# Kernel tuning notes

Measured on AMD Instinct MI355X. Metric: run time of the kernel, lower is better.

The kernel has to match this reference:

```python
import jax, jax.numpy as jnp
import numpy as np

C = 256; M = 8; K = 4; L = 4; DFF = 1024; CV = C // M
SHAPES = [(100, 100), (50, 50), (25, 25), (13, 13)]
B = 16; LQ = 900


def setup_inputs() -> dict:
    key = jax.random.key(0)
    ks = iter(jax.random.split(key, 64))
    def n(shape, s=0.02):
        return jax.random.normal(next(ks), shape, jnp.float32) * s
    inp = {
        "query_objects": n((LQ, B, C), 1.0),
        "query_poses": n((LQ, B, C), 1.0),
        "ref_points": jax.random.uniform(next(ks), (LQ, B, 2), jnp.float32),
    }
    for i, (h, w) in enumerate(SHAPES):
        inp[f"feat{i}"] = n((B, h, w, C), 1.0)
        inp[f"pos{i}"] = n((B, h, w, C), 1.0)
    inp.update(dict(
        sa_in_w=n((C, 3 * C)), sa_in_b=jnp.zeros((3 * C,), jnp.float32),
        sa_out_w=n((C, C)), sa_out_b=jnp.zeros((C,), jnp.float32),
        n1_g=jnp.ones((C,), jnp.float32), n1_b=jnp.zeros((C,), jnp.float32),
        n2_g=jnp.ones((C,), jnp.float32), n2_b=jnp.zeros((C,), jnp.float32),
        n3_g=jnp.ones((C,), jnp.float32), n3_b=jnp.zeros((C,), jnp.float32),
        val_w=n((C, C)), val_b=jnp.zeros((C,), jnp.float32),
        off_w=n((C, M * L * K * 2)), off_b=n((M * L * K * 2,), 0.5),
        aw_w=n((C, M * L * K)), aw_b=jnp.zeros((M * L * K,), jnp.float32),
        dout_w=n((C, C)), dout_b=jnp.zeros((C,), jnp.float32),
        ffn_w1=n((C, DFF)), ffn_b1=jnp.zeros((DFF,), jnp.float32),
        ffn_w2=n((DFF, C)), ffn_b2=jnp.zeros((C,), jnp.float32),
    ))
    return inp


def layernorm(x, g, b, eps=1e-5):
    m = x.mean(-1, keepdims=True)
    v = ((x - m) ** 2).mean(-1, keepdims=True)
    return (x - m) * jax.lax.rsqrt(v + eps) * g + b


def mha(x_q, x_k, x_v, Win, bin_, Wout, bout):
    # torch nn.MultiheadAttention, seq-first (Lq, B, C), no masks, eval mode
    Lq, Bn, _ = x_q.shape
    q = (x_q @ Win[:, :C] + bin_[:C]).reshape(Lq, Bn, M, CV)
    k = (x_k @ Win[:, C:2 * C] + bin_[C:2 * C]).reshape(Lq, Bn, M, CV)
    v = (x_v @ Win[:, 2 * C:] + bin_[2 * C:]).reshape(Lq, Bn, M, CV)
    a = jax.nn.softmax(jnp.einsum('qbmd,kbmd->bmqk', q * (CV ** -0.5), k), axis=-1)
    o = jnp.einsum('bmqk,kbmd->qbmd', a, v).reshape(Lq, Bn, C)
    return o @ Wout + bout


def deform_attn(qd, ref, feats, val_w, val_b, off_w, off_b, aw_w, aw_b, dout_w, dout_b):
    # qd: (B, Lq, C) queries; ref: (B, Lq, 2) normalized [0,1] reference points (x, y)
    Bn, Lq, _ = qd.shape
    off = (qd @ off_w + off_b).reshape(Bn, Lq, M, L, K, 2)            # sampling offsets (pixels)
    aw = jax.nn.softmax((qd @ aw_w + aw_b).reshape(Bn, Lq, M, L * K), axis=-1)
    aw = aw.reshape(Bn, Lq, M, L, K)                                   # attention weights over L*K
    out = jnp.zeros((Bn, Lq, M, CV), qd.dtype)
    for l, feat in enumerate(feats):
        H, W = feat.shape[1], feat.shape[2]
        # shared value projection, split into heads: (B, M, HW, Cv)
        v = (feat.reshape(Bn, H * W, C) @ val_w + val_b).reshape(Bn, H * W, M, CV).transpose(0, 2, 1, 3)
        px = ref[:, :, None, None, 0] * W - 0.5 + off[:, :, :, l, :, 0]  # (B, Lq, M, K)
        py = ref[:, :, None, None, 1] * H - 0.5 + off[:, :, :, l, :, 1]
        x0 = jnp.floor(px); y0 = jnp.floor(py)
        samp = jnp.zeros((Bn, M, Lq, K, CV), qd.dtype)
        for dx in (0.0, 1.0):
            for dy in (0.0, 1.0):
                xi = x0 + dx; yi = y0 + dy
                wgt = (1.0 - jnp.abs(px - xi)) * (1.0 - jnp.abs(py - yi))
                valid = (xi >= 0) & (xi < W) & (yi >= 0) & (yi < H)      # zero padding outside
                idx = (jnp.clip(yi, 0, H - 1) * W + jnp.clip(xi, 0, W - 1)).astype(jnp.int32)
                idx_t = idx.transpose(0, 2, 1, 3).reshape(Bn, M, Lq * K)
                g = jnp.take_along_axis(v, idx_t[..., None], axis=2).reshape(Bn, M, Lq, K, CV)
                samp = samp + g * (wgt * valid).transpose(0, 2, 1, 3)[..., None]
        out = out + jnp.einsum('bqmk,bmqkc->bqmc', aw[:, :, :, l], samp)
    return out.reshape(Bn, Lq, C) @ dout_w + dout_b


def reference(query_objects, query_poses, ref_points, feat0, feat1, feat2, feat3,
              pos0, pos1, pos2, pos3, sa_in_w, sa_in_b, sa_out_w, sa_out_b,
              n1_g, n1_b, n2_g, n2_b, n3_g, n3_b, val_w, val_b, off_w, off_b,
              aw_w, aw_b, dout_w, dout_b, ffn_w1, ffn_b1, ffn_w2, ffn_b2):
    # post-norm decoder layer, eval mode (dropout = identity)
    q = query_objects + query_poses
    x = query_objects + mha(q, q, query_objects, sa_in_w, sa_in_b, sa_out_w, sa_out_b)
    x = layernorm(x, n1_g, n1_b)
    feats = [feat0 + pos0, feat1 + pos1, feat2 + pos2, feat3 + pos3]
    qd = x.transpose(1, 0, 2)              # (B, Lq, C)
    ref = ref_points.transpose(1, 0, 2)    # (B, Lq, 2)
    d = deform_attn(qd, ref, feats, val_w, val_b, off_w, off_b, aw_w, aw_b, dout_w, dout_b)
    x = x + d.transpose(1, 0, 2)
    x = layernorm(x, n2_g, n2_b)
    x = x + (jax.nn.relu(x @ ffn_w1 + ffn_b1) @ ffn_w2 + ffn_b2)
    x = layernorm(x, n3_g, n3_b)
    return x
```

## Files before the change

kernel.cpp:

```cpp
#include <hip/hip_runtime.h>
#include <hip/hip_bf16.h>
#include <cstdint>

#define LQ 900
#define BB 16
#define CC 256
#define MM 8
#define CV 32
#define NROWS (LQ * BB)

typedef __attribute__((ext_vector_type(8))) short short8;
typedef __attribute__((ext_vector_type(4))) float f32x4;

__device__ __forceinline__ short f2bf(float f) {
    union { float f; unsigned u; } x; x.f = f;
    const unsigned r = x.u + 0x7fff + ((x.u >> 16) & 1);
    return (short)(r >> 16);
}
__device__ __forceinline__ float bf2f(ushort u) {
    union { unsigned u; float f; } c; c.u = ((unsigned)u) << 16; return c.f;
}

__device__ __constant__ int d_HW[4]    = {100, 50, 25, 13};
__device__ __constant__ int d_baseR[4] = {0, 160000, 200000, 210000};

__global__ __launch_bounds__(256) void conv_w_T(
    const float* __restrict__ W, ushort* __restrict__ Wt, int K, int N)
{
    __shared__ float tl[32][33];
    const int t = threadIdx.x;
    const int tx = t & 31, ty = t >> 5;
    const int n0 = blockIdx.x * 32, k0 = blockIdx.y * 32;
    #pragma unroll
    for (int p = 0; p < 4; ++p)
        tl[ty + 8 * p][tx] = W[(size_t)(k0 + ty + 8 * p) * N + n0 + tx];
    __syncthreads();
    #pragma unroll
    for (int p = 0; p < 4; ++p)
        Wt[(size_t)(n0 + ty + 8 * p) * K + k0 + tx] = (ushort)f2bf(tl[tx][ty + 8 * p]);
}

__global__ void concat_bias(const float* __restrict__ a, const float* __restrict__ b,
                            float* __restrict__ o)
{
    const int t = blockIdx.x * 256 + threadIdx.x;
    if (t < 384) o[t] = (t < 256) ? a[t] : b[t - 256];
}

#define EPS 136
#define LDSN 17408

template<bool A_BF16, bool ADD_A2, bool RELU, bool RESID, bool OUT_BF16>
__device__ __forceinline__ void gemm_core(
    ushort* lds,
    const void* __restrict__ Ap, const float* __restrict__ A2, int lda,
    const ushort* __restrict__ Bt, const float* __restrict__ bias,
    const float* __restrict__ resid, void* __restrict__ Cp, int ldc,
    int Mr, int Kd, int row0, int col0)
{
    ushort* As = lds;
    ushort* Bs = lds + 8192;

    const int t = threadIdx.x;
    const int lane = t & 63;
    const int w = t >> 6;
    const int wr = w >> 1, wc = w & 1;
    const int lr = lane & 15, lk = lane >> 4;

    f32x4 acc[4][4] = {};

    const int srow = t >> 4;
    const int skq  = (t & 15) * 4;
    const int sg   = (t & 15) >> 1;
    const int srem = (t & 1) * 8;

    const float*  Af = (const float*)Ap;
    const ushort* Ah = (const ushort*)Ap;

    short4 sa_[8], sb_[8];
    float4 fa_[8], f2_[8];

    const int nk = Kd >> 6;

    auto issue = [&](int kk0) {
        #pragma unroll
        for (int p = 0; p < 8; ++p) {
            const int gr = min(row0 + p * 16 + srow, Mr - 1);
            if constexpr (A_BF16) {
                sa_[p] = *reinterpret_cast<const short4*>(Ah + (size_t)gr * lda + kk0 + skq);
            } else {
                fa_[p] = *reinterpret_cast<const float4*>(Af + (size_t)gr * lda + kk0 + skq);
                if constexpr (ADD_A2)
                    f2_[p] = *reinterpret_cast<const float4*>(A2 + (size_t)gr * lda + kk0 + skq);
            }
            sb_[p] = *reinterpret_cast<const short4*>(Bt + (size_t)(col0 + p * 16 + srow) * Kd + kk0 + skq);
        }
    };

    issue(0);

    for (int kt = 0; kt < nk; ++kt) {
        #pragma unroll
        for (int p = 0; p < 8; ++p) {
            const int r = p * 16 + srow;
            short4 a4;
            if constexpr (A_BF16) {
                a4 = sa_[p];
            } else {
                float4 av = fa_[p];
                if constexpr (ADD_A2) {
                    av.x += f2_[p].x; av.y += f2_[p].y; av.z += f2_[p].z; av.w += f2_[p].w;
                }
                a4.x = f2bf(av.x); a4.y = f2bf(av.y); a4.z = f2bf(av.z); a4.w = f2bf(av.w);
            }
            const int byteA = r * 128 + ((sg ^ (r & 7)) << 4) + srem;
            *reinterpret_cast<short4*>((char*)As + byteA) = a4;
            *reinterpret_cast<short4*>((char*)Bs + byteA) = sb_[p];
        }
        __syncthreads();

        if (kt + 1 < nk) issue((kt + 1) * 64);

        #pragma unroll
        for (int kk = 0; kk < 2; ++kk) {
            short8 af[4], bfr[4];
            #pragma unroll
            for (int i = 0; i < 4; ++i) {
                const int r = wr * 64 + i * 16 + lr;
                const int byte = r * 128 + (((kk * 4 + lk) ^ (r & 7)) << 4);
                af[i] = *reinterpret_cast<const short8*>((char*)As + byte);
            }
            #pragma unroll
            for (int j = 0; j < 4; ++j) {
                const int r = wc * 64 + j * 16 + lr;
                const int byte = r * 128 + (((kk * 4 + lk) ^ (r & 7)) << 4);
                bfr[j] = *reinterpret_cast<const short8*>((char*)Bs + byte);
            }
            #pragma unroll
            for (int i = 0; i < 4; ++i)
                #pragma unroll
                for (int j = 0; j < 4; ++j)
                    acc[i][j] = __builtin_amdgcn_mfma_f32_16x16x32_bf16(af[i], bfr[j], acc[i][j], 0, 0, 0);
        }
        __syncthreads();
    }

    if constexpr (OUT_BF16) {
        ushort* Cb = (ushort*)Cp;
        #pragma unroll
        for (int j = 0; j < 4; ++j) {
            const int lcol = wc * 64 + j * 16 + lr;
            const float bcol = bias[col0 + lcol];
            #pragma unroll
            for (int i = 0; i < 4; ++i) {
                const int lrbase = wr * 64 + i * 16 + lk * 4;
                #pragma unroll
                for (int reg = 0; reg < 4; ++reg) {
                    float v = acc[i][j][reg] + bcol;
                    if (RELU) v = fmaxf(v, 0.f);
                    lds[(lrbase + reg) * EPS + lcol] = (ushort)f2bf(v);
                }
            }
        }
        __syncthreads();
        const int erow = t >> 1, ehalf = t & 1;
        if (row0 + erow < Mr) {
            ushort* dst = Cb + (size_t)(row0 + erow) * ldc + col0 + ehalf * 64;
            const ushort* src = lds + erow * EPS + ehalf * 64;
            #pragma unroll
            for (int q = 0; q < 8; ++q)
                *reinterpret_cast<short8*>(dst + q * 8) =
                    *reinterpret_cast<const short8*>(src + q * 8);
        }
    } else {
        float* Cf = (float*)Cp;
        #pragma unroll
        for (int j = 0; j < 4; ++j) {
            const int col = col0 + wc * 64 + j * 16 + lr;
            const float bcol = bias[col];
            #pragma unroll
            for (int i = 0; i < 4; ++i) {
                const int rbase = row0 + wr * 64 + i * 16 + lk * 4;
                #pragma unroll
                for (int reg = 0; reg < 4; ++reg) {
                    const int r = rbase + reg;
                    if (r < Mr) {
                        float v = acc[i][j][reg] + bcol;
                        if (RESID) v += resid[(size_t)r * ldc + col];
                        if (RELU)  v = fmaxf(v, 0.f);
                        Cf[(size_t)r * ldc + col] = v;
                    }
                }
            }
        }
    }
}

template<bool A_BF16, bool ADD_A2, bool RELU, bool RESID, bool OUT_BF16>
__global__ __launch_bounds__(256) void gemm_bf16(
    const void* __restrict__ Ap, const float* __restrict__ A2, int lda,
    const ushort* __restrict__ Bt, const float* __restrict__ bias,
    const float* __restrict__ resid, void* __restrict__ Cp, int ldc,
    int Mr, int Kd)
{
    __shared__ ushort lds[LDSN];
    gemm_core<A_BF16, ADD_A2, RELU, RESID, OUT_BF16>(
        lds, Ap, A2, lda, Bt, bias, resid, Cp, ldc, Mr, Kd,
        blockIdx.y * 128, blockIdx.x * 128);
}

__global__ __launch_bounds__(256) void attn_mfma(
    const ushort* __restrict__ QKbf, const ushort* __restrict__ Vbf,
    ushort* __restrict__ attnO)
{
    __shared__ ushort K_lds[64][40];
    __shared__ ushort Vt[32][72];
    __shared__ ushort P_lds[4][16][72];

    const int t = threadIdx.x;
    const int w = t >> 6, lane = t & 63;
    const int q0 = blockIdx.x * 64;
    const int m = blockIdx.y & 7, b = blockIdx.y >> 3;

    const int lr = lane & 15;
    const int lk = lane >> 4;

    const int qrow = min(q0 + w * 16 + lr, LQ - 1);
    const short8 qf = *reinterpret_cast<const short8*>(
        QKbf + ((size_t)qrow * BB + b) * 512 + m * 32 + lk * 8);

    f32x4 oacc[2] = {f32x4{0.f,0.f,0.f,0.f}, f32x4{0.f,0.f,0.f,0.f}};
    float mrun[4] = {-1e30f, -1e30f, -1e30f, -1e30f};
    float lrun[4] = {0.f, 0.f, 0.f, 0.f};

    const float scale = 0.17677669529663687f;
    const int sr = t >> 2;
    const int sd = (t & 3) * 8;

    for (int k0 = 0; k0 < LQ; k0 += 64) {
        {
            const int kr = min(k0 + sr, LQ - 1);
            *reinterpret_cast<short8*>(&K_lds[sr][sd]) =
                *reinterpret_cast<const short8*>(QKbf + ((size_t)kr * BB + b) * 512 + 256 + m * 32 + sd);
            const short8 v8 = *reinterpret_cast<const short8*>(
                Vbf + ((size_t)kr * BB + b) * 256 + m * 32 + sd);
            #pragma unroll
            for (int j = 0; j < 8; ++j) Vt[sd + j][sr] = (ushort)v8[j];
        }
        __syncthreads();

        f32x4 sa[4];
        #pragma unroll
        for (int n = 0; n < 4; ++n) {
            const short8 kf = *reinterpret_cast<const short8*>(&K_lds[n * 16 + lr][lk * 8]);
            sa[n] = __builtin_amdgcn_mfma_f32_16x16x32_bf16(qf, kf, f32x4{0.f,0.f,0.f,0.f}, 0, 0, 0);
        }
        #pragma unroll
        for (int n = 0; n < 4; ++n)
            #pragma unroll
            for (int r = 0; r < 4; ++r)
                sa[n][r] *= scale;
        if (k0 + 64 > LQ) {
            #pragma unroll
            for (int n = 0; n < 4; ++n)
                if (k0 + n * 16 + lr >= LQ) {
                    #pragma unroll
                    for (int r = 0; r < 4; ++r) sa[n][r] = -1e30f;
                }
        }

        #pragma unroll
        for (int r = 0; r < 4; ++r) {
            float mx = fmaxf(fmaxf(sa[0][r], sa[1][r]), fmaxf(sa[2][r], sa[3][r]));
            #pragma unroll
            for (int o = 8; o; o >>= 1) mx = fmaxf(mx, __shfl_xor(mx, o));
            const float mnew = fmaxf(mrun[r], mx);
            const float corr = __expf(mrun[r] - mnew);
            mrun[r] = mnew;
            float psum = 0.f;
            #pragma unroll
            for (int n = 0; n < 4; ++n) {
                const float p = __expf(sa[n][r] - mnew);
                psum += p;
                P_lds[w][lk * 4 + r][n * 16 + lr] = (ushort)f2bf(p);
            }
            #pragma unroll
            for (int o = 8; o; o >>= 1) psum += __shfl_xor(psum, o);
            lrun[r] = lrun[r] * corr + psum;
            oacc[0][r] *= corr;
            oacc[1][r] *= corr;
        }

        #pragma unroll
        for (int kk = 0; kk < 2; ++kk) {
            const short8 pf = *reinterpret_cast<const short8*>(&P_lds[w][lr][kk * 32 + lk * 8]);
            #pragma unroll
            for (int dt = 0; dt < 2; ++dt) {
                const short8 vf = *reinterpret_cast<const short8*>(&Vt[dt * 16 + lr][kk * 32 + lk * 8]);
                oacc[dt] = __builtin_amdgcn_mfma_f32_16x16x32_bf16(pf, vf, oacc[dt], 0, 0, 0);
            }
        }
        __syncthreads();
    }

    #pragma unroll
    for (int r = 0; r < 4; ++r) {
        const int row = q0 + w * 16 + lk * 4 + r;
        if (row < LQ) {
            const float inv = 1.f / lrun[r];
            ushort* op = attnO + ((size_t)row * BB + b) * 256 + m * 32;
            op[lr]      = (ushort)f2bf(oacc[0][r] * inv);
            op[16 + lr] = (ushort)f2bf(oacc[1][r] * inv);
        }
    }
}

__global__ __launch_bounds__(256) void ln_kernel(
    const float* __restrict__ X, const float* __restrict__ g,
    const float* __restrict__ bta, float* __restrict__ Y, int nrows)
{
    const int r = blockIdx.x * 4 + (threadIdx.x >> 6);
    if (r >= nrows) return;
    const int lane = threadIdx.x & 63;
    const float4 v = *reinterpret_cast<const float4*>(X + (size_t)r * 256 + lane * 4);
    float s  = v.x + v.y + v.z + v.w;
    float sq = v.x * v.x + v.y * v.y + v.z * v.z + v.w * v.w;
    #pragma unroll
    for (int o = 32; o; o >>= 1) { s += __shfl_xor(s, o); sq += __shfl_xor(sq, o); }
    const float mean = s * (1.f / 256.f);
    const float var  = sq * (1.f / 256.f) - mean * mean;
    const float rs   = rsqrtf(var + 1e-5f);
    const float4 gv = *reinterpret_cast<const float4*>(g + lane * 4);
    const float4 bv = *reinterpret_cast<const float4*>(bta + lane * 4);
    float4 o4;
    o4.x = (v.x - mean) * rs * gv.x + bv.x;
    o4.y = (v.y - mean) * rs * gv.y + bv.y;
    o4.z = (v.z - mean) * rs * gv.z + bv.z;
    o4.w = (v.w - mean) * rs * gv.w + bv.w;
    *reinterpret_cast<float4*>(Y + (size_t)r * 256 + lane * 4) = o4;
}

__global__ __launch_bounds__(256) void samp_prep(
    const float* __restrict__ ref, const float* __restrict__ obf,
    int4* __restrict__ prepI, float4* __restrict__ prepW)
{
    const int gid = blockIdx.x * 256 + threadIdx.x;
    const int k = gid & 3, l = (gid >> 2) & 3, m = (gid >> 4) & 7, row = gid >> 7;
    const int b = row & 15;

    const float logit = obf[(size_t)row * 384 + 256 + m * 16 + l * 4 + k];
    float mx = logit;
    #pragma unroll
    for (int o = 1; o < 16; o <<= 1) mx = fmaxf(mx, __shfl_xor(mx, o));
    const float e = __expf(logit - mx);
    float se = e;
    #pragma unroll
    for (int o = 1; o < 16; o <<= 1) se += __shfl_xor(se, o);
    const float aw = e / se;

    const int   Hl = d_HW[l];
    const float Hf = (float)Hl;
    const int   gbase = d_baseR[l] + b * Hl * Hl;
    const float rx = ref[row * 2 + 0], ry = ref[row * 2 + 1];
    const float ox = obf[(size_t)row * 384 + m * 32 + l * 8 + k * 2 + 0];
    const float oy = obf[(size_t)row * 384 + m * 32 + l * 8 + k * 2 + 1];
    const float px = rx * Hf - 0.5f + ox;
    const float py = ry * Hf - 0.5f + oy;
    const float x0 = floorf(px), y0 = floorf(py);

    int4 I; float4 W;
    #pragma unroll
    for (int c = 0; c < 4; ++c) {
        const float xi = x0 + (float)(c & 1);
        const float yi = y0 + (float)(c >> 1);
        const float wv = (1.f - fabsf(px - xi)) * (1.f - fabsf(py - yi));
        const bool valid = (xi >= 0.f) && (xi < Hf) && (yi >= 0.f) && (yi < Hf);
        const int ix = min(max((int)xi, 0), Hl - 1);
        const int iy = min(max((int)yi, 0), Hl - 1);
        const int idx = gbase + iy * Hl + ix;
        const float wgt = valid ? aw * wv : 0.f;
        if (c == 0) { I.x = idx; W.x = wgt; }
        else if (c == 1) { I.y = idx; W.y = wgt; }
        else if (c == 2) { I.z = idx; W.z = wgt; }
        else { I.w = idx; W.w = wgt; }
    }
    prepI[gid] = I;
    prepW[gid] = W;
}

__global__ __launch_bounds__(256) void samp_gather(
    const ushort* __restrict__ Vval, const int4* __restrict__ prepI,
    const float4* __restrict__ prepW, float* __restrict__ samp)
{
    const int wid  = blockIdx.x * 4 + (threadIdx.x >> 6);
    const int lane = threadIdx.x & 63;
    const int q  = wid % LQ;
    const int bm = wid / LQ;
    const int m  = bm & 7, b = bm >> 3;
    const int row = q * BB + b;
    const int sid = lane >> 3, dg = lane & 7;

    const uint2* V4 = (const uint2*)Vval;
    const int pbase = (row * 8 + m) * 16;
    const int coff  = m * 8 + dg;

    float a0 = 0.f, a1 = 0.f, a2 = 0.f, a3 = 0.f;
    #pragma unroll
    for (int g = 0; g < 2; ++g) {
        const int s = g * 8 + sid;
        const int4   I = prepI[pbase + s];
        const float4 W = prepW[pbase + s];
        uint2 v;
        v = V4[(size_t)I.x * 64 + coff];
        a0 += W.x * bf2f((ushort)v.x); a1 += W.x * bf2f((ushort)(v.x >> 16));
        a2 += W.x * bf2f((ushort)v.y); a3 += W.x * bf2f((ushort)(v.y >> 16));
        v = V4[(size_t)I.y * 64 + coff];
        a0 += W.y * bf2f((ushort)v.x); a1 += W.y * bf2f((ushort)(v.x >> 16));
        a2 += W.y * bf2f((ushort)v.y); a3 += W.y * bf2f((ushort)(v.y >> 16));
        v = V4[(size_t)I.z * 64 + coff];
        a0 += W.z * bf2f((ushort)v.x); a1 += W.z * bf2f((ushort)(v.x >> 16));
        a2 += W.z * bf2f((ushort)v.y); a3 += W.z * bf2f((ushort)(v.y >> 16));
        v = V4[(size_t)I.w * 64 + coff];
        a0 += W.w * bf2f((ushort)v.x); a1 += W.w * bf2f((ushort)(v.x >> 16));
        a2 += W.w * bf2f((ushort)v.y); a3 += W.w * bf2f((ushort)(v.y >> 16));
    }
    #pragma unroll
    for (int o = 8; o <= 32; o <<= 1) {
        a0 += __shfl_xor(a0, o); a1 += __shfl_xor(a1, o);
        a2 += __shfl_xor(a2, o); a3 += __shfl_xor(a3, o);
    }
    if (sid == 0) {
        float4 o4; o4.x = a0; o4.y = a1; o4.z = a2; o4.w = a3;
        *reinterpret_cast<float4*>(samp + (size_t)row * 256 + m * 32 + dg * 4) = o4;
    }
}

extern "C" void kernel_launch(void* const* d_in, const int* in_sizes, int n_in,
                              void* d_out, int out_size, void* d_ws, size_t ws_size,
                              hipStream_t stream)
{
    const float* qo   = (const float*)d_in[0];
    const float* qpz  = (const float*)d_in[1];
    const float* refp = (const float*)d_in[2];
    const float* feat[4] = {(const float*)d_in[3], (const float*)d_in[5],
                            (const float*)d_in[7], (const float*)d_in[9]};
    const float* pos[4]  = {(const float*)d_in[4], (const float*)d_in[6],
                            (const float*)d_in[8], (const float*)d_in[10]};
    const float* sa_in_w  = (const float*)d_in[11];
    const float* sa_in_b  = (const float*)d_in[12];
    const float* sa_out_w = (const float*)d_in[13];
    const float* sa_out_b = (const float*)d_in[14];
    const float* n1_g = (const float*)d_in[15];
    const float* n1_b = (const float*)d_in[16];
    const float* n2_g = (const float*)d_in[17];
    const float* n2_b = (const float*)d_in[18];
    const float* n3_g = (const float*)d_in[19];
    const float* n3_b = (const float*)d_in[20];
    const float* val_w  = (const float*)d_in[21];
    const float* val_b  = (const float*)d_in[22];
    const float* off_w  = (const float*)d_in[23];
    const float* off_b  = (const float*)d_in[24];
    const float* aw_w   = (const float*)d_in[25];
    const float* aw_b   = (const float*)d_in[26];
    const float* dout_w = (const float*)d_in[27];
    const float* dout_b = (const float*)d_in[28];
    const float* ffn_w1 = (const float*)d_in[29];
    const float* ffn_b1 = (const float*)d_in[30];
    const float* ffn_w2 = (const float*)d_in[31];
    const float* ffn_b2 = (const float*)d_in[32];

    char* ws = (char*)d_ws;
    ushort* QKbf   = (ushort*)(ws + 0);
    ushort* Vbf    = (ushort*)(ws + 14745600);
    ushort* attnO  = (ushort*)(ws + 22118400);
    ushort* Vval   = (ushort*)(ws + 29491200);
    ushort* WsaInT = (ushort*)(ws + 138395648);
    ushort* WsaOutT= (ushort*)(ws + 138788864);
    ushort* WvalT  = (ushort*)(ws + 138919936);
    ushort* WdoutT = (ushort*)(ws + 139051008);
    ushort* Wffn1T = (ushort*)(ws + 139182080);
    ushort* Wffn2T = (ushort*)(ws + 139706368);
    ushort* WoffAwT= (ushort*)(ws + 140230656);
    float*  obias  = (float*)(ws + 140427264);
    float* x1   = (float*)(ws + 140429312);
    float* dres = x1;
    float* xln1 = (float*)(ws + 155174912);
    float* obf  = (float*)(ws + 169920512);
    float* x3   = obf;
    float* samp = (float*)(ws + 192038912);
    float* xln2 = (float*)(ws + 206784512);
    ushort* h   = (ushort*)(ws + 221530112);
    int4*  prepI = (int4*)(ws + 251021312);
    float4* prepW = (float4*)(ws + 280512512);

    const dim3 blk(256);
    const int GM = (NROWS + 127) / 128;

    conv_w_T<<<dim3(24, 8), blk, 0, stream>>>(sa_in_w, WsaInT, 256, 768);
    conv_w_T<<<dim3(8, 8), blk, 0, stream>>>(sa_out_w, WsaOutT, 256, 256);
    conv_w_T<<<dim3(8, 8), blk, 0, stream>>>(val_w, WvalT, 256, 256);
    conv_w_T<<<dim3(8, 8), blk, 0, stream>>>(dout_w, WdoutT, 256, 256);
    conv_w_T<<<dim3(32, 8), blk, 0, stream>>>(ffn_w1, Wffn1T, 256, 1024);
    conv_w_T<<<dim3(8, 32), blk, 0, stream>>>(ffn_w2, Wffn2T, 1024, 256);
    conv_w_T<<<dim3(8, 8), blk, 0, stream>>>(off_w, WoffAwT, 256, 256);
    conv_w_T<<<dim3(4, 8), blk, 0, stream>>>(aw_w, WoffAwT + 256 * 256, 256, 128);
    concat_bias<<<dim3(2), blk, 0, stream>>>(off_b, aw_b, obias);

    gemm_bf16<false, true, false, false, true><<<dim3(4, GM), blk, 0, stream>>>(
        qo, qpz, 256, WsaInT, sa_in_b, nullptr, QKbf, 512, NROWS, 256);
    gemm_bf16<false, false, false, false, true><<<dim3(2, GM), blk, 0, stream>>>(
        qo, nullptr, 256, WsaInT + 512 * 256, sa_in_b + 512, nullptr, Vbf, 256, NROWS, 256);
    attn_mfma<<<dim3(15, 128), blk, 0, stream>>>(QKbf, Vbf, attnO);
    gemm_bf16<true, false, false, true, false><<<dim3(2, GM), blk, 0, stream>>>(
        attnO, nullptr, 256, WsaOutT, sa_out_b, qo, x1, 256, NROWS, 256);
    ln_kernel<<<dim3(3600), blk, 0, stream>>>(x1, n1_g, n1_b, xln1, NROWS);
    gemm_bf16<false, false, false, false, false><<<dim3(3, GM), blk, 0, stream>>>(
        xln1, nullptr, 256, WoffAwT, obias, nullptr, obf, 384, NROWS, 256);
    samp_prep<<<dim3(7200), blk, 0, stream>>>(refp, obf, prepI, prepW);
    gemm_bf16<false, true, false, false, true><<<dim3(2, 1250), blk, 0, stream>>>(
        feat[0], pos[0], 256, WvalT, val_b, nullptr, Vval, 256, 160000, 256);
    gemm_bf16<false, true, false, false, true><<<dim3(2, 313), blk, 0, stream>>>(
        feat[1], pos[1], 256, WvalT, val_b, nullptr, Vval + (size_t)160000 * 256, 256, 40000, 256);
    gemm_bf16<false, true, false, false, true><<<dim3(2, 79), blk, 0, stream>>>(
        feat[2], pos[2], 256, WvalT, val_b, nullptr, Vval + (size_t)200000 * 256, 256, 10000, 256);
    gemm_bf16<false, true, false, false, true><<<dim3(2, 22), blk, 0, stream>>>(
        feat[3], pos[3], 256, WvalT, val_b, nullptr, Vval + (size_t)210000 * 256, 256, 2704, 256);
    samp_gather<<<dim3(28800), blk, 0, stream>>>(Vval, prepI, prepW, samp);
    gemm_bf16<false, false, false, true, false><<<dim3(2, GM), blk, 0, stream>>>(
        samp, nullptr, 256, WdoutT, dout_b, xln1, dres, 256, NROWS, 256);
    ln_kernel<<<dim3(3600), blk, 0, stream>>>(dres, n2_g, n2_b, xln2, NROWS);
    gemm_bf16<false, false, true, false, true><<<dim3(8, GM), blk, 0, stream>>>(
        xln2, nullptr, 256, Wffn1T, ffn_b1, nullptr, h, 1024, NROWS, 256);
    gemm_bf16<true, false, false, true, false><<<dim3(2, GM), blk, 0, stream>>>(
        h, nullptr, 1024, Wffn2T, ffn_b2, xln2, x3, 256, NROWS, 1024);
    ln_kernel<<<dim3(3600), blk, 0, stream>>>(x3, n3_g, n3_b, (float*)d_out, NROWS);
}
```

Before: 600.0 us.

## Merge weight conversion launches, fuse sampling prep into gather, store intermediates in bf16

All weight transpose/convert launches and the bias concat are folded into one kernel that looks up its work item through a packed descriptor. The sampling-prep kernel is removed: each gather wavefront now computes its own softmax weights and bilinear indices into LDS, so the prepI/prepW buffers no longer go through global memory. LayerNorm outputs and the sampled features are stored as bf16, and the downstream GEMMs read bf16 A operands and bf16 residuals. This cuts launch count and global traffic, at the cost of extra rounding on the residual paths.

New measurement: 529.2 us. 1.13x faster.

```diff
diff --git a/kernel.cpp b/kernel.cpp
--- a/kernel.cpp
+++ b/kernel.cpp
@@ -24,38 +24,57 @@
 __device__ __constant__ int d_HW[4]    = {100, 50, 25, 13};
 __device__ __constant__ int d_baseR[4] = {0, 160000, 200000, 210000};
 
-__global__ __launch_bounds__(256) void conv_w_T(
-    const float* __restrict__ W, ushort* __restrict__ Wt, int K, int N)
-{
+struct WPack {
+    const float* W[8];
+    ushort*      Wt[8];
+    int K[8];
+    int N[8];
+    int cum[9];
+    const float* offb;
+    const float* awb;
+    float*       obias;
+};
+
+__global__ __launch_bounds__(256) void conv_all(WPack p)
+{
+    const int bb = blockIdx.x;
+    if (bb == p.cum[8]) {
+        for (int t = threadIdx.x; t < 384; t += 256)
+            p.obias[t] = (t < 256) ? p.offb[t] : p.awb[t - 256];
+        return;
+    }
+    int wi = 0;
+    #pragma unroll
+    for (int i = 0; i < 8; ++i)
+        if (bb >= p.cum[i + 1]) wi = i + 1;
+    const int ti  = bb - p.cum[wi];
+    const int N   = p.N[wi], K = p.K[wi];
+    const int ntx = N >> 5;
+    const int n0  = (ti % ntx) * 32, k0 = (ti / ntx) * 32;
+    const float* W  = p.W[wi];
+    ushort*      Wt = p.Wt[wi];
+
     __shared__ float tl[32][33];
     const int t = threadIdx.x;
     const int tx = t & 31, ty = t >> 5;
-    const int n0 = blockIdx.x * 32, k0 = blockIdx.y * 32;
-    #pragma unroll
-    for (int p = 0; p < 4; ++p)
-        tl[ty + 8 * p][tx] = W[(size_t)(k0 + ty + 8 * p) * N + n0 + tx];
+    #pragma unroll
+    for (int q = 0; q < 4; ++q)
+        tl[ty + 8 * q][tx] = W[(size_t)(k0 + ty + 8 * q) * N + n0 + tx];
     __syncthreads();
     #pragma unroll
-    for (int p = 0; p < 4; ++p)
-        Wt[(size_t)(n0 + ty + 8 * p) * K + k0 + tx] = (ushort)f2bf(tl[tx][ty + 8 * p]);
-}
-
-__global__ void concat_bias(const float* __restrict__ a, const float* __restrict__ b,
-                            float* __restrict__ o)
-{
-    const int t = blockIdx.x * 256 + threadIdx.x;
-    if (t < 384) o[t] = (t < 256) ? a[t] : b[t - 256];
+    for (int q = 0; q < 4; ++q)
+        Wt[(size_t)(n0 + ty + 8 * q) * K + k0 + tx] = (ushort)f2bf(tl[tx][ty + 8 * q]);
 }
 
 #define EPS 136
 #define LDSN 17408
 
-template<bool A_BF16, bool ADD_A2, bool RELU, bool RESID, bool OUT_BF16>
+template<bool A_BF16, bool ADD_A2, bool RELU, bool RESID, bool RESID_BF16, bool OUT_BF16>
 __device__ __forceinline__ void gemm_core(
     ushort* lds,
     const void* __restrict__ Ap, const float* __restrict__ A2, int lda,
     const ushort* __restrict__ Bt, const float* __restrict__ bias,
-    const float* __restrict__ resid, void* __restrict__ Cp, int ldc,
+    const void* __restrict__ resid, void* __restrict__ Cp, int ldc,
     int Mr, int Kd, int row0, int col0)
 {
     ushort* As = lds;
@@ -186,8 +205,13 @@
                     const int r = rbase + reg;
                     if (r < Mr) {
                         float v = acc[i][j][reg] + bcol;
-                        if (RESID) v += resid[(size_t)r * ldc + col];
-                        if (RELU)  v = fmaxf(v, 0.f);
+                        if (RESID) {
+                            if (RESID_BF16)
+                                v += bf2f(((const ushort*)resid)[(size_t)r * ldc + col]);
+                            else
+                                v += ((const float*)resid)[(size_t)r * ldc + col];
+                        }
+                        if (RELU) v = fmaxf(v, 0.f);
                         Cf[(size_t)r * ldc + col] = v;
                     }
                 }
@@ -196,15 +220,15 @@
     }
 }
 
-template<bool A_BF16, bool ADD_A2, bool RELU, bool RESID, bool OUT_BF16>
+template<bool A_BF16, bool ADD_A2, bool RELU, bool RESID, bool RESID_BF16, bool OUT_BF16>
 __global__ __launch_bounds__(256) void gemm_bf16(
     const void* __restrict__ Ap, const float* __restrict__ A2, int lda,
     const ushort* __restrict__ Bt, const float* __restrict__ bias,
-    const float* __restrict__ resid, void* __restrict__ Cp, int ldc,
+    const void* __restrict__ resid, void* __restrict__ Cp, int ldc,
     int Mr, int Kd)
 {
     __shared__ ushort lds[LDSN];
-    gemm_core<A_BF16, ADD_A2, RELU, RESID, OUT_BF16>(
+    gemm_core<A_BF16, ADD_A2, RELU, RESID, RESID_BF16, OUT_BF16>(
         lds, Ap, A2, lda, Bt, bias, resid, Cp, ldc, Mr, Kd,
         blockIdx.y * 128, blockIdx.x * 128);
 }
@@ -315,9 +339,10 @@
     }
 }
 
+template<bool OUT_BF16>
 __global__ __launch_bounds__(256) void ln_kernel(
     const float* __restrict__ X, const float* __restrict__ g,
-    const float* __restrict__ bta, float* __restrict__ Y, int nrows)
+    const float* __restrict__ bta, void* __restrict__ Y, int nrows)
 {
     const int r = blockIdx.x * 4 + (threadIdx.x >> 6);
     if (r >= nrows) return;
@@ -337,79 +362,75 @@
     o4.y = (v.y - mean) * rs * gv.y + bv.y;
     o4.z = (v.z - mean) * rs * gv.z + bv.z;
     o4.w = (v.w - mean) * rs * gv.w + bv.w;
-    *reinterpret_cast<float4*>(Y + (size_t)r * 256 + lane * 4) = o4;
-}
-
-__global__ __launch_bounds__(256) void samp_prep(
-    const float* __restrict__ ref, const float* __restrict__ obf,
-    int4* __restrict__ prepI, float4* __restrict__ prepW)
-{
-    const int gid = blockIdx.x * 256 + threadIdx.x;
-    const int k = gid & 3, l = (gid >> 2) & 3, m = (gid >> 4) & 7, row = gid >> 7;
-    const int b = row & 15;
-
-    const float logit = obf[(size_t)row * 384 + 256 + m * 16 + l * 4 + k];
-    float mx = logit;
-    #pragma unroll
-    for (int o = 1; o < 16; o <<= 1) mx = fmaxf(mx, __shfl_xor(mx, o));
-    const float e = __expf(logit - mx);
-    float se = e;
-    #pragma unroll
-    for (int o = 1; o < 16; o <<= 1) se += __shfl_xor(se, o);
-    const float aw = e / se;
-
-    const int   Hl = d_HW[l];
-    const float Hf = (float)Hl;
-    const int   gbase = d_baseR[l] + b * Hl * Hl;
-    const float rx = ref[row * 2 + 0], ry = ref[row * 2 + 1];
-    const float ox = obf[(size_t)row * 384 + m * 32 + l * 8 + k * 2 + 0];
-    const float oy = obf[(size_t)row * 384 + m * 32 + l * 8 + k * 2 + 1];
-    const float px = rx * Hf - 0.5f + ox;
-    const float py = ry * Hf - 0.5f + oy;
-    const float x0 = floorf(px), y0 = floorf(py);
-
-    int4 I; float4 W;
-    #pragma unroll
-    for (int c = 0; c < 4; ++c) {
-        const float xi = x0 + (float)(c & 1);
-        const float yi = y0 + (float)(c >> 1);
-        const float wv = (1.f - fabsf(px - xi)) * (1.f - fabsf(py - yi));
-        const bool valid = (xi >= 0.f) && (xi < Hf) && (yi >= 0.f) && (yi < Hf);
-        const int ix = min(max((int)xi, 0), Hl - 1);
-        const int iy = min(max((int)yi, 0), Hl - 1);
-        const int idx = gbase + iy * Hl + ix;
-        const float wgt = valid ? aw * wv : 0.f;
-        if (c == 0) { I.x = idx; W.x = wgt; }
-        else if (c == 1) { I.y = idx; W.y = wgt; }
-        else if (c == 2) { I.z = idx; W.z = wgt; }
-        else { I.w = idx; W.w = wgt; }
-    }
-    prepI[gid] = I;
-    prepW[gid] = W;
+    if (OUT_BF16) {
+        short4 u;
+        u.x = f2bf(o4.x); u.y = f2bf(o4.y); u.z = f2bf(o4.z); u.w = f2bf(o4.w);
+        *reinterpret_cast<short4*>((ushort*)Y + (size_t)r * 256 + lane * 4) = u;
+    } else {
+        *reinterpret_cast<float4*>((float*)Y + (size_t)r * 256 + lane * 4) = o4;
+    }
 }
 
 __global__ __launch_bounds__(256) void samp_gather(
-    const ushort* __restrict__ Vval, const int4* __restrict__ prepI,
-    const float4* __restrict__ prepW, float* __restrict__ samp)
-{
-    const int wid  = blockIdx.x * 4 + (threadIdx.x >> 6);
+    const ushort* __restrict__ Vval, const float* __restrict__ obf,
+    const float* __restrict__ ref, ushort* __restrict__ samp)
+{
+    __shared__ int   sI[4][16][4];
+    __shared__ float sW[4][16][4];
+
+    const int w    = threadIdx.x >> 6;
     const int lane = threadIdx.x & 63;
+    const int wid  = blockIdx.x * 4 + w;
     const int q  = wid % LQ;
     const int bm = wid / LQ;
     const int m  = bm & 7, b = bm >> 3;
     const int row = q * BB + b;
+
+    if (lane < 16) {
+        const float logit = obf[(size_t)row * 384 + 256 + m * 16 + lane];
+        float mx = logit;
+        #pragma unroll
+        for (int o = 1; o < 16; o <<= 1) mx = fmaxf(mx, __shfl_xor(mx, o));
+        const float e = __expf(logit - mx);
+        float se = e;
+        #pragma unroll
+        for (int o = 1; o < 16; o <<= 1) se += __shfl_xor(se, o);
+        const float aw = e / se;
+
+        const int   l  = lane >> 2;
+        const int   Hl = d_HW[l];
+        const float Hf = (float)Hl;
+        const int   gbase = d_baseR[l] + b * Hl * Hl;
+        const float rx = ref[row * 2 + 0], ry = ref[row * 2 + 1];
+        const float ox = obf[(size_t)row * 384 + m * 32 + lane * 2 + 0];
+        const float oy = obf[(size_t)row * 384 + m * 32 + lane * 2 + 1];
+        const float px = rx * Hf - 0.5f + ox;
+        const float py = ry * Hf - 0.5f + oy;
+        const float x0 = floorf(px), y0 = floorf(py);
+
+        #pragma unroll
+        for (int c = 0; c < 4; ++c) {
+            const float xi = x0 + (float)(c & 1);
+            const float yi = y0 + (float)(c >> 1);
+            const float wv = (1.f - fabsf(px - xi)) * (1.f - fabsf(py - yi));
+            const bool valid = (xi >= 0.f) && (xi < Hf) && (yi >= 0.f) && (yi < Hf);
+            const int ix = min(max((int)xi, 0), Hl - 1);
+            const int iy = min(max((int)yi, 0), Hl - 1);
+            sI[w][lane][c] = gbase + iy * Hl + ix;
+            sW[w][lane][c] = valid ? aw * wv : 0.f;
+        }
+    }
+
     const int sid = lane >> 3, dg = lane & 7;
-
     const uint2* V4 = (const uint2*)Vval;
-    const int pbase = (row * 8 + m) * 16;
     const int coff  = m * 8 + dg;
 
     float a0 = 0.f, a1 = 0.f, a2 = 0.f, a3 = 0.f;
     #pragma unroll
     for (int g = 0; g < 2; ++g) {
         const int s = g * 8 + sid;
-        const int4   I = prepI[pbase + s];
-        const float4 W = prepW[pbase + s];
+        const int4   I = *reinterpret_cast<const int4*>(&sI[w][s][0]);
+        const float4 W = *reinterpret_cast<const float4*>(&sW[w][s][0]);
         uint2 v;
         v = V4[(size_t)I.x * 64 + coff];
         a0 += W.x * bf2f((ushort)v.x); a1 += W.x * bf2f((ushort)(v.x >> 16));
@@ -430,8 +451,9 @@
         a2 += __shfl_xor(a2, o); a3 += __shfl_xor(a3, o);
     }
     if (sid == 0) {
-        float4 o4; o4.x = a0; o4.y = a1; o4.z = a2; o4.w = a3;
-        *reinterpret_cast<float4*>(samp + (size_t)row * 256 + m * 32 + dg * 4) = o4;
+        short4 u;
+        u.x = f2bf(a0); u.y = f2bf(a1); u.z = f2bf(a2); u.w = f2bf(a3);
+        *reinterpret_cast<short4*>(samp + (size_t)row * 256 + m * 32 + dg * 4) = u;
     }
 }
 
@@ -482,56 +504,57 @@
     ushort* Wffn2T = (ushort*)(ws + 139706368);
     ushort* WoffAwT= (ushort*)(ws + 140230656);
     float*  obias  = (float*)(ws + 140427264);
-    float* x1   = (float*)(ws + 140429312);
-    float* dres = x1;
-    float* xln1 = (float*)(ws + 155174912);
-    float* obf  = (float*)(ws + 169920512);
-    float* x3   = obf;
-    float* samp = (float*)(ws + 192038912);
-    float* xln2 = (float*)(ws + 206784512);
-    ushort* h   = (ushort*)(ws + 221530112);
-    int4*  prepI = (int4*)(ws + 251021312);
-    float4* prepW = (float4*)(ws + 280512512);
+    float*  x1   = (float*)(ws + 140429312);
+    float*  dres = x1;
+    ushort* xln1 = (ushort*)(ws + 155174912);
+    float*  obf  = (float*)(ws + 162547712);
+    ushort* samp = (ushort*)(ws + 184666112);
+    ushort* xln2 = (ushort*)(ws + 192038912);
+    ushort* h    = (ushort*)(ws + 199411712);
+    float*  x3   = (float*)(ws + 228902912);
 
     const dim3 blk(256);
     const int GM = (NROWS + 127) / 128;
 
-    conv_w_T<<<dim3(24, 8), blk, 0, stream>>>(sa_in_w, WsaInT, 256, 768);
-    conv_w_T<<<dim3(8, 8), blk, 0, stream>>>(sa_out_w, WsaOutT, 256, 256);
-    conv_w_T<<<dim3(8, 8), blk, 0, stream>>>(val_w, WvalT, 256, 256);
-    conv_w_T<<<dim3(8, 8), blk, 0, stream>>>(dout_w, WdoutT, 256, 256);
-    conv_w_T<<<dim3(32, 8), blk, 0, stream>>>(ffn_w1, Wffn1T, 256, 1024);
-    conv_w_T<<<dim3(8, 32), blk, 0, stream>>>(ffn_w2, Wffn2T, 1024, 256);
-    conv_w_T<<<dim3(8, 8), blk, 0, stream>>>(off_w, WoffAwT, 256, 256);
-    conv_w_T<<<dim3(4, 8), blk, 0, stream>>>(aw_w, WoffAwT + 256 * 256, 256, 128);
-    concat_bias<<<dim3(2), blk, 0, stream>>>(off_b, aw_b, obias);
-
-    gemm_bf16<false, true, false, false, true><<<dim3(4, GM), blk, 0, stream>>>(
+    WPack wp;
+    wp.W[0] = sa_in_w;  wp.Wt[0] = WsaInT;  wp.K[0] = 256;  wp.N[0] = 768;
+    wp.W[1] = sa_out_w; wp.Wt[1] = WsaOutT; wp.K[1] = 256;  wp.N[1] = 256;
+    wp.W[2] = val_w;    wp.Wt[2] = WvalT;   wp.K[2] = 256;  wp.N[2] = 256;
+    wp.W[3] = dout_w;   wp.Wt[3] = WdoutT;  wp.K[3] = 256;  wp.N[3] = 256;
+    wp.W[4] = ffn_w1;   wp.Wt[4] = Wffn1T;  wp.K[4] = 256;  wp.N[4] = 1024;
+    wp.W[5] = ffn_w2;   wp.Wt[5] = Wffn2T;  wp.K[5] = 1024; wp.N[5] = 256;
+    wp.W[6] = off_w;    wp.Wt[6] = WoffAwT; wp.K[6] = 256;  wp.N[6] = 256;
+    wp.W[7] = aw_w;     wp.Wt[7] = WoffAwT + 256 * 256; wp.K[7] = 256; wp.N[7] = 128;
+    const int cums[9] = {0, 192, 256, 320, 384, 640, 896, 960, 992};
+    for (int i = 0; i < 9; ++i) wp.cum[i] = cums[i];
+    wp.offb = off_b; wp.awb = aw_b; wp.obias = obias;
+    conv_all<<<dim3(993), blk, 0, stream>>>(wp);
+
+    gemm_bf16<false, true, false, false, false, true><<<dim3(4, GM), blk, 0, stream>>>(
         qo, qpz, 256, WsaInT, sa_in_b, nullptr, QKbf, 512, NROWS, 256);
-    gemm_bf16<false, false, false, false, true><<<dim3(2, GM), blk, 0, stream>>>(
+    gemm_bf16<false, false, false, false, false, true><<<dim3(2, GM), blk, 0, stream>>>(
         qo, nullptr, 256, WsaInT + 512 * 256, sa_in_b + 512, nullptr, Vbf, 256, NROWS, 256);
     attn_mfma<<<dim3(15, 128), blk, 0, stream>>>(QKbf, Vbf, attnO);
-    gemm_bf16<true, false, false, true, false><<<dim3(2, GM), blk, 0, stream>>>(
+    gemm_bf16<true, false, false, true, false, false><<<dim3(2, GM), blk, 0, stream>>>(
         attnO, nullptr, 256, WsaOutT, sa_out_b, qo, x1, 256, NROWS, 256);
-    ln_kernel<<<dim3(3600), blk, 0, stream>>>(x1, n1_g, n1_b, xln1, NROWS);
-    gemm_bf16<false, false, false, false, false><<<dim3(3, GM), blk, 0, stream>>>(
+    ln_kernel<true><<<dim3(3600), blk, 0, stream>>>(x1, n1_g, n1_b, xln1, NROWS);
+    gemm_bf16<true, false, false, false, false, false><<<dim3(3, GM), blk, 0, stream>>>(
         xln1, nullptr, 256, WoffAwT, obias, nullptr, obf, 384, NROWS, 256);
-    samp_prep<<<dim3(7200), blk, 0, stream>>>(refp, obf, prepI, prepW);
-    gemm_bf16<false, true, false, false, true><<<dim3(2, 1250), blk, 0, stream>>>(
+    gemm_bf16<false, true, false, false, false, true><<<dim3(2, 1250), blk, 0, stream>>>(
         feat[0], pos[0], 256, WvalT, val_b, nullptr, Vval, 256, 160000, 256);
-    gemm_bf16<false, true, false, false, true><<<dim3(2, 313), blk, 0, stream>>>(
+    gemm_bf16<false, true, false, false, false, true><<<dim3(2, 313), blk, 0, stream>>>(
         feat[1], pos[1], 256, WvalT, val_b, nullptr, Vval + (size_t)160000 * 256, 256, 40000, 256);
-    gemm_bf16<false, true, false, false, true><<<dim3(2, 79), blk, 0, stream>>>(
+    gemm_bf16<false, true, false, false, false, true><<<dim3(2, 79), blk, 0, stream>>>(
         feat[2], pos[2], 256, WvalT, val_b, nullptr, Vval + (size_t)200000 * 256, 256, 10000, 256);
-    gemm_bf16<false, true, false, false, true><<<dim3(2, 22), blk, 0, stream>>>(
+    gemm_bf16<false, true, false, false, false, true><<<dim3(2, 22), blk, 0, stream>>>(
         feat[3], pos[3], 256, WvalT, val_b, nullptr, Vval + (size_t)210000 * 256, 256, 2704, 256);
-    samp_gather<<<dim3(28800), blk, 0, stream>>>(Vval, prepI, prepW, samp);
-    gemm_bf16<false, false, false, true, false><<<dim3(2, GM), blk, 0, stream>>>(
+    samp_gather<<<dim3(28800), blk, 0, stream>>>(Vval, obf, refp, samp);
+    gemm_bf16<true, false, false, true, true, false><<<dim3(2, GM), blk, 0, stream>>>(
         samp, nullptr, 256, WdoutT, dout_b, xln1, dres, 256, NROWS, 256);
-    ln_kernel<<<dim3(3600), blk, 0, stream>>>(dres, n2_g, n2_b, xln2, NROWS);
-    gemm_bf16<false, false, true, false, true><<<dim3(8, GM), blk, 0, stream>>>(
+    ln_kernel<true><<<dim3(3600), blk, 0, stream>>>(dres, n2_g, n2_b, xln2, NROWS);
+    gemm_bf16<true, false, true, false, false, true><<<dim3(8, GM), blk, 0, stream>>>(
         xln2, nullptr, 256, Wffn1T, ffn_b1, nullptr, h, 1024, NROWS, 256);
-    gemm_bf16<true, false, false, true, false><<<dim3(2, GM), blk, 0, stream>>>(
+    gemm_bf16<true, false, false, true, true, false><<<dim3(2, GM), blk, 0, stream>>>(
         h, nullptr, 1024, Wffn2T, ffn_b2, xln2, x3, 256, NROWS, 1024);
-    ln_kernel<<<dim3(3600), blk, 0, stream>>>(x3, n3_g, n3_b, (float*)d_out, NROWS);
-}
+    ln_kernel<false><<<dim3(3600), blk, 0, stream>>>(x3, n3_g, n3_b, (float*)d_out, NROWS);
+}
```
